# Kernel tuning notes

Hardware: AMD Instinct MI355X
Metric: run time of the kernel (lower is better)

## Reference

```python
import jax, jax.numpy as jnp
import numpy as np

LAMBDA_LAME = 1.0
MU_LAME = 0.5
JACOBIAN_WEIGHT = 0.1
ERROR_BOUND = 0.01


def setup_inputs() -> dict:
    key = jax.random.key(0)
    df = jax.random.normal(key, (2, 3, 192, 192, 192), dtype=jnp.float32)
    return {"deformation_field": df}


def _grad(x, axis):
    # matches torch.gradient / np.gradient (edge_order=1): central diff in the
    # interior, one-sided first-order at the boundaries, unit spacing.
    return jnp.gradient(x, axis=axis)


def _robust(x, delta):
    abs_x = jnp.abs(x)
    return jnp.where(abs_x <= delta, 0.5 * x * x, delta * (abs_x - 0.5 * delta))


def reference(deformation_field):
    u = deformation_field[:, 0]  # [B, D, H, W]
    v = deformation_field[:, 1]
    w = deformation_field[:, 2]

    du_dx, du_dy, du_dz = _grad(u, 1), _grad(u, 2), _grad(u, 3)
    dv_dx, dv_dy, dv_dz = _grad(v, 1), _grad(v, 2), _grad(v, 3)
    dw_dx, dw_dy, dw_dz = _grad(w, 1), _grad(w, 2), _grad(w, 3)

    E_xx, E_yy, E_zz = du_dx, dv_dy, dw_dz
    E_xy = 0.5 * (du_dy + dv_dx)
    E_xz = 0.5 * (du_dz + dw_dx)
    E_yz = 0.5 * (dv_dz + dw_dy)
    trace_E = E_xx + E_yy + E_zz

    d = ERROR_BOUND
    tr_l = _robust(trace_E, d)
    energy = (0.5 * LAMBDA_LAME * tr_l ** 2
              + MU_LAME * (_robust(E_xx, d) ** 2 + _robust(E_yy, d) ** 2
                           + _robust(E_zz, d) ** 2
                           + 2.0 * (_robust(E_xy, d) ** 2
                                    + _robust(E_xz, d) ** 2
                                    + _robust(E_yz, d) ** 2)))

    jac = ((1 + du_dx) * ((1 + dv_dy) * (1 + dw_dz) - dv_dz * dw_dy)
           - du_dy * (dv_dx * (1 + dw_dz) - dv_dz * (1 + dw_dx))
           + du_dz * (dv_dx * dw_dy - (1 + dv_dy) * (1 + dw_dx)))
    jac_penalty = jax.nn.relu(-jac)

    total = jnp.mean(energy) + JACOBIAN_WEIGHT * jnp.mean(jac_penalty)
    return total
```

## Files before the change

kernel.cpp:

```cpp
#include <hip/hip_runtime.h>

#define DIM 192
#define PLANE (DIM * DIM)
#define VOL ((size_t)PLANE * DIM)
#define NTOT (2.0 * 7077888.0)

__device__ __forceinline__ float robustf(float x) {
    float ax = fabsf(x);
    return (ax <= 0.01f) ? (0.5f * x * x) : (0.01f * (ax - 0.005f));
}

__global__ __launch_bounds__(256)
void elastic_main(const float* __restrict__ df, double* __restrict__ acc) {
    const int tx = threadIdx.x;
    const int k = (blockIdx.x % 3) * 64 + (tx & 63);
    const int j = (blockIdx.x / 3) * 4 + (tx >> 6);
    const int i0 = blockIdx.y * 24;
    const int b = blockIdx.z;

    const float* __restrict__ u = df + (size_t)(b * 3 + 0) * VOL;
    const float* __restrict__ v = df + (size_t)(b * 3 + 1) * VOL;
    const float* __restrict__ w = df + (size_t)(b * 3 + 2) * VOL;

    const int jp = (j < DIM - 1) ? j + 1 : j;
    const int jm = (j > 0) ? j - 1 : j;
    const int kp = (k < DIM - 1) ? k + 1 : k;
    const int km = (k > 0) ? k - 1 : k;
    const float sy = ((jp - jm) == 2) ? 0.5f : 1.0f;
    const float sz = ((kp - km) == 2) ? 0.5f : 1.0f;

    float vsum = 0.0f;

    for (int ii = 0; ii < 24; ++ii) {
        const int i = i0 + ii;
        const int ip = (i < DIM - 1) ? i + 1 : i;
        const int im = (i > 0) ? i - 1 : i;
        const float sx = ((ip - im) == 2) ? 0.5f : 1.0f;

        const size_t rowC  = (size_t)i  * PLANE + (size_t)j  * DIM;
        const size_t rowXp = (size_t)ip * PLANE + (size_t)j  * DIM;
        const size_t rowXm = (size_t)im * PLANE + (size_t)j  * DIM;
        const size_t rowYp = (size_t)i  * PLANE + (size_t)jp * DIM;
        const size_t rowYm = (size_t)i  * PLANE + (size_t)jm * DIM;

        const float du_dx = (u[rowXp + k] - u[rowXm + k]) * sx;
        const float dv_dx = (v[rowXp + k] - v[rowXm + k]) * sx;
        const float dw_dx = (w[rowXp + k] - w[rowXm + k]) * sx;
        const float du_dy = (u[rowYp + k] - u[rowYm + k]) * sy;
        const float dv_dy = (v[rowYp + k] - v[rowYm + k]) * sy;
        const float dw_dy = (w[rowYp + k] - w[rowYm + k]) * sy;
        const float du_dz = (u[rowC + kp] - u[rowC + km]) * sz;
        const float dv_dz = (v[rowC + kp] - v[rowC + km]) * sz;
        const float dw_dz = (w[rowC + kp] - w[rowC + km]) * sz;

        const float E_xy = 0.5f * (du_dy + dv_dx);
        const float E_xz = 0.5f * (du_dz + dw_dx);
        const float E_yz = 0.5f * (dv_dz + dw_dy);
        const float tr   = du_dx + dv_dy + dw_dz;

        const float rtr = robustf(tr);
        const float rxx = robustf(du_dx), ryy = robustf(dv_dy), rzz = robustf(dw_dz);
        const float rxy = robustf(E_xy),  rxz = robustf(E_xz),  ryz = robustf(E_yz);

        const float energy = 0.5f * rtr * rtr
                           + 0.5f * (rxx * rxx + ryy * ryy + rzz * rzz
                                     + 2.0f * (rxy * rxy + rxz * rxz + ryz * ryz));

        const float jac =
              (1.0f + du_dx) * ((1.0f + dv_dy) * (1.0f + dw_dz) - dv_dz * dw_dy)
            - du_dy * (dv_dx * (1.0f + dw_dz) - dv_dz * (1.0f + dw_dx))
            + du_dz * (dv_dx * dw_dy - (1.0f + dv_dy) * (1.0f + dw_dx));

        vsum += energy + 0.1f * fmaxf(-jac, 0.0f);
    }

    #pragma unroll
    for (int off = 32; off > 0; off >>= 1)
        vsum += __shfl_down(vsum, off, 64);

    __shared__ float wpart[4];
    if ((tx & 63) == 0) wpart[tx >> 6] = vsum;
    __syncthreads();
    if (tx == 0) {
        double s = (double)wpart[0] + (double)wpart[1]
                 + (double)wpart[2] + (double)wpart[3];
        unsafeAtomicAdd(acc, s);
    }
}

__global__ void elastic_finalize(const double* __restrict__ acc, float* __restrict__ out) {
    out[0] = (float)(acc[0] * (1.0 / NTOT));
}

extern "C" void kernel_launch(void* const* d_in, const int* in_sizes, int n_in,
                              void* d_out, int out_size, void* d_ws, size_t ws_size,
                              hipStream_t stream) {
    const float* df = (const float*)d_in[0];
    double* acc = (double*)d_ws;
    float* out = (float*)d_out;

    hipMemsetAsync(d_ws, 0, sizeof(double), stream);

    dim3 grid(144, 8, 2);
    elastic_main<<<grid, 256, 0, stream>>>(df, acc);
    elastic_finalize<<<1, 1, 0, stream>>>(acc, out);
}
```

Baseline: 261.3 us.

## Vectorize stencil loads with float4 and share z-neighbors via wave shuffles

```diff
diff --git a/kernel.cpp b/kernel.cpp
--- a/kernel.cpp
+++ b/kernel.cpp
@@ -3,20 +3,60 @@
 #define DIM 192
 #define PLANE (DIM * DIM)
 #define VOL ((size_t)PLANE * DIM)
-#define NTOT (2.0 * 7077888.0)
+#define NTOT (2.0 * 14155776.0 / 2.0)
 
 __device__ __forceinline__ float robustf(float x) {
     float ax = fabsf(x);
     return (ax <= 0.01f) ? (0.5f * x * x) : (0.01f * (ax - 0.005f));
 }
 
+__device__ __forceinline__ float4 ldg4(const float* __restrict__ p) {
+    return *(const float4*)p;
+}
+
+__device__ __forceinline__ float voxel_loss(
+    float du_dx, float du_dy, float du_dz,
+    float dv_dx, float dv_dy, float dv_dz,
+    float dw_dx, float dw_dy, float dw_dz) {
+    const float E_xy = 0.5f * (du_dy + dv_dx);
+    const float E_xz = 0.5f * (du_dz + dw_dx);
+    const float E_yz = 0.5f * (dv_dz + dw_dy);
+    const float tr   = du_dx + dv_dy + dw_dz;
+
+    const float rtr = robustf(tr);
+    const float rxx = robustf(du_dx), ryy = robustf(dv_dy), rzz = robustf(dw_dz);
+    const float rxy = robustf(E_xy),  rxz = robustf(E_xz),  ryz = robustf(E_yz);
+
+    const float energy = 0.5f * rtr * rtr
+                       + 0.5f * (rxx * rxx + ryy * ryy + rzz * rzz
+                                 + 2.0f * (rxy * rxy + rxz * rxz + ryz * ryz));
+
+    const float jac =
+          (1.0f + du_dx) * ((1.0f + dv_dy) * (1.0f + dw_dz) - dv_dz * dw_dy)
+        - du_dy * (dv_dx * (1.0f + dw_dz) - dv_dz * (1.0f + dw_dx))
+        + du_dz * (dv_dx * dw_dy - (1.0f + dv_dy) * (1.0f + dw_dx));
+
+    return energy + 0.1f * fmaxf(-jac, 0.0f);
+}
+
+__device__ __forceinline__ float4 zgrad(float4 c, float lf, float rt,
+                                        bool leftEdge, bool rightEdge) {
+    float4 g;
+    g.x = leftEdge  ? (c.y - c.x) : 0.5f * (c.y - lf);
+    g.y = 0.5f * (c.z - c.x);
+    g.z = 0.5f * (c.w - c.y);
+    g.w = rightEdge ? (c.w - c.z) : 0.5f * (rt - c.z);
+    return g;
+}
+
 __global__ __launch_bounds__(256)
 void elastic_main(const float* __restrict__ df, double* __restrict__ acc) {
     const int tx = threadIdx.x;
-    const int k = (blockIdx.x % 3) * 64 + (tx & 63);
-    const int j = (blockIdx.x / 3) * 4 + (tx >> 6);
-    const int i0 = blockIdx.y * 24;
-    const int b = blockIdx.z;
+    const int ty = threadIdx.y;
+    const int k4 = tx * 4;
+    const int j  = blockIdx.x * 4 + ty;
+    const int i0 = blockIdx.y * 16;
+    const int b  = blockIdx.z;
 
     const float* __restrict__ u = df + (size_t)(b * 3 + 0) * VOL;
     const float* __restrict__ v = df + (size_t)(b * 3 + 1) * VOL;
@@ -24,54 +64,81 @@
 
     const int jp = (j < DIM - 1) ? j + 1 : j;
     const int jm = (j > 0) ? j - 1 : j;
-    const int kp = (k < DIM - 1) ? k + 1 : k;
-    const int km = (k > 0) ? k - 1 : k;
     const float sy = ((jp - jm) == 2) ? 0.5f : 1.0f;
-    const float sz = ((kp - km) == 2) ? 0.5f : 1.0f;
+
+    const bool act = (tx < 48);
+    const bool leftEdge  = (tx == 0);
+    const bool rightEdge = (tx == 47);
 
     float vsum = 0.0f;
 
-    for (int ii = 0; ii < 24; ++ii) {
+    for (int ii = 0; ii < 16; ++ii) {
         const int i = i0 + ii;
         const int ip = (i < DIM - 1) ? i + 1 : i;
         const int im = (i > 0) ? i - 1 : i;
         const float sx = ((ip - im) == 2) ? 0.5f : 1.0f;
 
-        const size_t rowC  = (size_t)i  * PLANE + (size_t)j  * DIM;
-        const size_t rowXp = (size_t)ip * PLANE + (size_t)j  * DIM;
-        const size_t rowXm = (size_t)im * PLANE + (size_t)j  * DIM;
-        const size_t rowYp = (size_t)i  * PLANE + (size_t)jp * DIM;
-        const size_t rowYm = (size_t)i  * PLANE + (size_t)jm * DIM;
+        const size_t oC  = (size_t)i  * PLANE + (size_t)j  * DIM + k4;
+        const size_t oXp = (size_t)ip * PLANE + (size_t)j  * DIM + k4;
+        const size_t oXm = (size_t)im * PLANE + (size_t)j  * DIM + k4;
+        const size_t oYp = (size_t)i  * PLANE + (size_t)jp * DIM + k4;
+        const size_t oYm = (size_t)i  * PLANE + (size_t)jm * DIM + k4;
 
-        const float du_dx = (u[rowXp + k] - u[rowXm + k]) * sx;
-        const float dv_dx = (v[rowXp + k] - v[rowXm + k]) * sx;
-        const float dw_dx = (w[rowXp + k] - w[rowXm + k]) * sx;
-        const float du_dy = (u[rowYp + k] - u[rowYm + k]) * sy;
-        const float dv_dy = (v[rowYp + k] - v[rowYm + k]) * sy;
-        const float dw_dy = (w[rowYp + k] - w[rowYm + k]) * sy;
-        const float du_dz = (u[rowC + kp] - u[rowC + km]) * sz;
-        const float dv_dz = (v[rowC + kp] - v[rowC + km]) * sz;
-        const float dw_dz = (w[rowC + kp] - w[rowC + km]) * sz;
+        float4 uc, vc, wc;
+        float4 uxp, uxm, vxp, vxm, wxp, wxm;
+        float4 uyp, uym, vyp, vym, wyp, wym;
 
-        const float E_xy = 0.5f * (du_dy + dv_dx);
-        const float E_xz = 0.5f * (du_dz + dw_dx);
-        const float E_yz = 0.5f * (dv_dz + dw_dy);
-        const float tr   = du_dx + dv_dy + dw_dz;
+        if (act) {
+            uc  = ldg4(u + oC);  vc  = ldg4(v + oC);  wc  = ldg4(w + oC);
+            uxp = ldg4(u + oXp); uxm = ldg4(u + oXm);
+            vxp = ldg4(v + oXp); vxm = ldg4(v + oXm);
+            wxp = ldg4(w + oXp); wxm = ldg4(w + oXm);
+            uyp = ldg4(u + oYp); uym = ldg4(u + oYm);
+            vyp = ldg4(v + oYp); vym = ldg4(v + oYm);
+            wyp = ldg4(w + oYp); wym = ldg4(w + oYm);
+        } else {
+            uc = vc = wc = make_float4(0.f, 0.f, 0.f, 0.f);
+        }
 
-        const float rtr = robustf(tr);
-        const float rxx = robustf(du_dx), ryy = robustf(dv_dy), rzz = robustf(dw_dz);
-        const float rxy = robustf(E_xy),  rxz = robustf(E_xz),  ryz = robustf(E_yz);
+        const float ulf = __shfl_up(uc.w, 1);
+        const float vlf = __shfl_up(vc.w, 1);
+        const float wlf = __shfl_up(wc.w, 1);
+        const float urt = __shfl_down(uc.x, 1);
+        const float vrt = __shfl_down(vc.x, 1);
+        const float wrt = __shfl_down(wc.x, 1);
 
-        const float energy = 0.5f * rtr * rtr
-                           + 0.5f * (rxx * rxx + ryy * ryy + rzz * rzz
-                                     + 2.0f * (rxy * rxy + rxz * rxz + ryz * ryz));
+        if (act) {
+            const float4 du_dz = zgrad(uc, ulf, urt, leftEdge, rightEdge);
+            const float4 dv_dz = zgrad(vc, vlf, vrt, leftEdge, rightEdge);
+            const float4 dw_dz = zgrad(wc, wlf, wrt, leftEdge, rightEdge);
 
-        const float jac =
-              (1.0f + du_dx) * ((1.0f + dv_dy) * (1.0f + dw_dz) - dv_dz * dw_dy)
-            - du_dy * (dv_dx * (1.0f + dw_dz) - dv_dz * (1.0f + dw_dx))
-            + du_dz * (dv_dx * dw_dy - (1.0f + dv_dy) * (1.0f + dw_dx));
+            float4 du_dx, dv_dx, dw_dx, du_dy, dv_dy, dw_dy;
+            du_dx.x = (uxp.x - uxm.x) * sx; du_dx.y = (uxp.y - uxm.y) * sx;
+            du_dx.z = (uxp.z - uxm.z) * sx; du_dx.w = (uxp.w - uxm.w) * sx;
+            dv_dx.x = (vxp.x - vxm.x) * sx; dv_dx.y = (vxp.y - vxm.y) * sx;
+            dv_dx.z = (vxp.z - vxm.z) * sx; dv_dx.w = (vxp.w - vxm.w) * sx;
+            dw_dx.x = (wxp.x - wxm.x) * sx; dw_dx.y = (wxp.y - wxm.y) * sx;
+            dw_dx.z = (wxp.z - wxm.z) * sx; dw_dx.w = (wxp.w - wxm.w) * sx;
+            du_dy.x = (uyp.x - uym.x) * sy; du_dy.y = (uyp.y - uym.y) * sy;
+            du_dy.z = (uyp.z - uym.z) * sy; du_dy.w = (uyp.w - uym.w) * sy;
+            dv_dy.x = (vyp.x - vym.x) * sy; dv_dy.y = (vyp.y - vym.y) * sy;
+            dv_dy.z = (vyp.z - vym.z) * sy; dv_dy.w = (vyp.w - vym.w) * sy;
+            dw_dy.x = (wyp.x - wym.x) * sy; dw_dy.y = (wyp.y - wym.y) * sy;
+            dw_dy.z = (wyp.z - wym.z) * sy; dw_dy.w = (wyp.w - wym.w) * sy;
 
-        vsum += energy + 0.1f * fmaxf(-jac, 0.0f);
+            vsum += voxel_loss(du_dx.x, du_dy.x, du_dz.x,
+                               dv_dx.x, dv_dy.x, dv_dz.x,
+                               dw_dx.x, dw_dy.x, dw_dz.x);
+            vsum += voxel_loss(du_dx.y, du_dy.y, du_dz.y,
+                               dv_dx.y, dv_dy.y, dv_dz.y,
+                               dw_dx.y, dw_dy.y, dw_dz.y);
+            vsum += voxel_loss(du_dx.z, du_dy.z, du_dz.z,
+                               dv_dx.z, dv_dy.z, dv_dz.z,
+                               dw_dx.z, dw_dy.z, dw_dz.z);
+            vsum += voxel_loss(du_dx.w, du_dy.w, du_dz.w,
+                               dv_dx.w, dv_dy.w, dv_dz.w,
+                               dw_dx.w, dw_dy.w, dw_dz.w);
+        }
     }
 
     #pragma unroll
@@ -79,9 +146,9 @@
         vsum += __shfl_down(vsum, off, 64);
 
     __shared__ float wpart[4];
-    if ((tx & 63) == 0) wpart[tx >> 6] = vsum;
+    if (tx == 0) wpart[ty] = vsum;
     __syncthreads();
-    if (tx == 0) {
+    if (tx == 0 && ty == 0) {
         double s = (double)wpart[0] + (double)wpart[1]
                  + (double)wpart[2] + (double)wpart[3];
         unsafeAtomicAdd(acc, s);
@@ -89,7 +156,7 @@
 }
 
 __global__ void elastic_finalize(const double* __restrict__ acc, float* __restrict__ out) {
-    out[0] = (float)(acc[0] * (1.0 / NTOT));
+    out[0] = (float)(acc[0] * (1.0 / 14155776.0));
 }
 
 extern "C" void kernel_launch(void* const* d_in, const int* in_sizes, int n_in,
@@ -101,7 +168,8 @@
 
     hipMemsetAsync(d_ws, 0, sizeof(double), stream);
 
-    dim3 grid(144, 8, 2);
-    elastic_main<<<grid, 256, 0, stream>>>(df, acc);
+    dim3 grid(48, 12, 2);
+    dim3 block(64, 4);
+    elastic_main<<<grid, block, 0, stream>>>(df, acc);
     elastic_finalize<<<1, 1, 0, stream>>>(acc, out);
 }
```

Result: no change. 261.4 us (+0.0%).
